# Performance work log

Hardware: AMD Instinct MI355X
Metric: run time of the kernel (lower is better)

## Reference

```python
import jax, jax.numpy as jnp
import numpy as np

NV, NK, DK, DV, KC = 32, 16, 128, 128, 4  # value heads, key heads, head dims, conv kernel
EPS = 1e-6


def setup_inputs() -> dict:
    key = jax.random.key(0)
    ks = jax.random.split(key, 10)
    B, T, D = 2, 4096, 2048
    key_dim, value_dim = NK * DK, NV * DV
    conv_dim = 2 * key_dim + value_dim
    s = 0.02
    return {
        "hidden_states": jax.random.normal(ks[0], (B, T, D), jnp.float32),
        "W_qkv": jax.random.normal(ks[1], (D, conv_dim), jnp.float32) * s,
        "W_z": jax.random.normal(ks[2], (D, value_dim), jnp.float32) * s,
        "W_b": jax.random.normal(ks[3], (D, NV), jnp.float32) * s,
        "W_a": jax.random.normal(ks[4], (D, NV), jnp.float32) * s,
        "conv_w": jax.random.normal(ks[5], (conv_dim, KC), jnp.float32) * 0.2,
        "dt_bias": jnp.ones((NV,), jnp.float32),
        "A_log": jnp.log(jax.random.uniform(ks[6], (NV,), jnp.float32, 0.5, 16.0)),
        "norm_w": jnp.ones((DV,), jnp.float32),
        "W_out": jax.random.normal(ks[7], (value_dim, D), jnp.float32) * s,
    }


def _silu(x):
    return x * jax.nn.sigmoid(x)


def _l2norm(x):
    return x * jax.lax.rsqrt(jnp.sum(x * x, axis=-1, keepdims=True) + EPS)


def _gated_delta_rule(q, k, v, g, beta):
    # q,k: [B,T,H,DK]; v: [B,T,H,DV]; g,beta: [B,T,H]
    tm = lambda x: jnp.moveaxis(x, 1, 0)  # time-major
    B, T, H = q.shape[0], q.shape[1], q.shape[2]
    S0 = jnp.zeros((B, H, q.shape[-1], v.shape[-1]), q.dtype)

    def step(S, xs):
        qt, kt, vt, gt, bt = xs
        S = S * jnp.exp(gt)[..., None, None]                       # decay
        kS = jnp.einsum('bhk,bhkv->bhv', kt, S)                    # k^T S
        S = S + bt[..., None, None] * kt[..., :, None] * (vt - kS)[..., None, :]
        o = jnp.einsum('bhk,bhkv->bhv', qt, S)
        return S, o

    _, o = jax.lax.scan(step, S0, (tm(q), tm(k), tm(v), tm(g), tm(beta)))
    return jnp.moveaxis(o, 0, 1)  # [B,T,H,DV]


def reference(hidden_states, W_qkv, W_z, W_b, W_a, conv_w, dt_bias, A_log, norm_w, W_out):
    B, T, D = hidden_states.shape
    key_dim, value_dim = NK * DK, NV * DV

    mixed = hidden_states @ W_qkv                                  # [B,T,conv_dim]
    z = (hidden_states @ W_z).reshape(B, T, NV, DV)
    beta = jax.nn.sigmoid(hidden_states @ W_b)                     # [B,T,NV]
    a = hidden_states @ W_a
    g = -jnp.exp(A_log) * jax.nn.softplus(a + dt_bias)             # [B,T,NV]

    # causal depthwise short conv (kernel KC) + silu
    xp = jnp.pad(mixed, ((0, 0), (KC - 1, 0), (0, 0)))
    conv = sum(xp[:, i:i + T, :] * conv_w[:, i] for i in range(KC))
    mixed = _silu(conv)

    q, k, v = jnp.split(mixed, [key_dim, 2 * key_dim], axis=-1)
    q = q.reshape(B, T, NK, DK)
    k = k.reshape(B, T, NK, DK)
    v = v.reshape(B, T, NV, DV)
    rep = NV // NK
    q = jnp.repeat(q, rep, axis=2)
    k = jnp.repeat(k, rep, axis=2)

    q = _l2norm(q) * (DK ** -0.5)
    k = _l2norm(k)

    o = _gated_delta_rule(q, k, v, g, beta)                        # [B,T,NV,DV]

    # fused gated RMSNorm: rmsnorm(o)*w * silu(z)
    var = jnp.mean(o * o, axis=-1, keepdims=True)
    o = o * jax.lax.rsqrt(var + 1e-6) * norm_w * _silu(z)

    return o.reshape(B, T, value_dim) @ W_out
```

## Files before the change

### kernel.cpp

```cpp
#include <hip/hip_runtime.h>
#include <hip/hip_bf16.h>


typedef __attribute__((ext_vector_type(8))) short short8;
typedef __attribute__((ext_vector_type(4))) float f32x4;
typedef unsigned short us;

static __device__ __forceinline__ us f2b(float f) {
  __hip_bfloat16 h = __float2bfloat16(f);
  return __builtin_bit_cast(us, h);
}
static __device__ __forceinline__ float b2f(us u) {
  return __bfloat162float(__builtin_bit_cast(__hip_bfloat16, u));
}
static __device__ __forceinline__ void bar_lds() {
  asm volatile("s_waitcnt lgkmcnt(0)" ::: "memory");
  __builtin_amdgcn_s_barrier();
}

__global__ __launch_bounds__(256) void cvt_f32_bf16(const float* __restrict__ in,
    us* __restrict__ out, long n4) {
  long i = (long)blockIdx.x * 256 + threadIdx.x;
  long stride = (long)gridDim.x * 256;
  for (; i < n4; i += stride) {
    float4 f = reinterpret_cast<const float4*>(in)[i];
    ushort4 u;
    u.x = f2b(f.x); u.y = f2b(f.y); u.z = f2b(f.z); u.w = f2b(f.w);
    reinterpret_cast<ushort4*>(out)[i] = u;
  }
}

__global__ __launch_bounds__(256) void transpose_cvt(const float* __restrict__ in,
    us* __restrict__ out, int K, int N, int Nfull, int coloff, int row_off) {
  __shared__ float tile[64][65];
  int tid = threadIdx.x;
  int n0 = blockIdx.x * 64, k0 = blockIdx.y * 64;
  int tx = tid & 15, ty = tid >> 4;
#pragma unroll
  for (int r = 0; r < 4; ++r) {
    int kk = k0 + ty + r * 16, nn = n0 + tx * 4;
    float4 v = make_float4(0.f, 0.f, 0.f, 0.f);
    if (kk < K && nn < N)
      v = *reinterpret_cast<const float4*>(in + (size_t)kk * Nfull + coloff + nn);
    tile[ty + r * 16][tx * 4 + 0] = v.x;
    tile[ty + r * 16][tx * 4 + 1] = v.y;
    tile[ty + r * 16][tx * 4 + 2] = v.z;
    tile[ty + r * 16][tx * 4 + 3] = v.w;
  }
  __syncthreads();
#pragma unroll
  for (int g = 0; g < 2; ++g) {
    int s = tid + g * 256;
    int nn = s >> 3, ks = (s & 7) * 8;
    if (n0 + nn < N && k0 + ks < K) {
      us ov[8];
#pragma unroll
      for (int i = 0; i < 8; ++i) ov[i] = f2b(tile[ks + i][nn]);
      *reinterpret_cast<uint4*>(out + (size_t)(n0 + nn + row_off) * K + k0 + ks) =
          *reinterpret_cast<uint4*>(ov);
    }
  }
}

template <bool BF16OUT>
__global__ __launch_bounds__(512, 1) void gemm256(const us* __restrict__ A,
    const us* __restrict__ B, void* __restrict__ Cout, int K, int ldC) {
  __shared__ us Abuf[2][256 * 64];
  __shared__ us Bbuf[2][256 * 64];
  int tid = threadIdx.x, w = tid >> 6, lane = tid & 63;
  int wr = w >> 2, wc = w & 3;
  int fr = lane & 15, j4 = lane >> 4;
  int lin = blockIdx.y * gridDim.x + blockIdx.x;
  int nwg = gridDim.x * gridDim.y;
  int wg = (lin & 7) * (nwg >> 3) + (lin >> 3);
  int bx = wg % gridDim.x, by = wg / gridDim.x;
  size_t bm = (size_t)bx * 256, bn = (size_t)by * 256;

  const us *aG[4], *bG[4];
  us *aL[2][4], *bL[2][4];
#pragma unroll
  for (int u = 0; u < 4; ++u) {
    int idx = u * 512 + tid;
    int row = idx >> 3, sl = idx & 7;
    int sg = (sl ^ (row & 7)) * 8;
    aG[u] = A + (bm + row) * K + sg;
    bG[u] = B + (bn + row) * K + sg;
    int lbase = (u * 64 + w * 8) * 64;
#pragma unroll
    for (int bf = 0; bf < 2; ++bf) {
      aL[bf][u] = &Abuf[bf][lbase];
      bL[bf][u] = &Bbuf[bf][lbase];
    }
  }

  f32x4 acc[8][4] = {};
#pragma unroll
  for (int u = 0; u < 4; ++u) {
    __builtin_amdgcn_global_load_lds((const void*)aG[u], (void*)aL[0][u], 16, 0, 0);
    __builtin_amdgcn_global_load_lds((const void*)bG[u], (void*)bL[0][u], 16, 0, 0);
  }
  __syncthreads();

  int nt = K >> 6;
  for (int t = 0; t < nt; ++t) {
    int cur = t & 1, nxt = cur ^ 1;
    const us* Ac = Abuf[cur];
    const us* Bc = Bbuf[cur];
    int kt1 = (t + 1) << 6;
    bool more = (t + 1 < nt);
#pragma unroll
    for (int q = 0; q < 4; ++q) {
      if (more) {
        __builtin_amdgcn_global_load_lds((const void*)(aG[q] + kt1), (void*)aL[nxt][q], 16, 0, 0);
        __builtin_amdgcn_global_load_lds((const void*)(bG[q] + kt1), (void*)bL[nxt][q], 16, 0, 0);
      }
      short8 a0[2], a1[2], bfv[4][2];
      int Ra0 = wr * 128 + 2 * q * 16 + fr;
      int Ra1 = Ra0 + 16;
#pragma unroll
      for (int ks = 0; ks < 2; ++ks) {
        a0[ks] = *reinterpret_cast<const short8*>(&Ac[Ra0 * 64 + (((ks * 4 + j4) ^ (Ra0 & 7)) * 8)]);
        a1[ks] = *reinterpret_cast<const short8*>(&Ac[Ra1 * 64 + (((ks * 4 + j4) ^ (Ra1 & 7)) * 8)]);
#pragma unroll
        for (int fj = 0; fj < 4; ++fj) {
          int Rb = wc * 64 + fj * 16 + fr;
          bfv[fj][ks] = *reinterpret_cast<const short8*>(&Bc[Rb * 64 + (((ks * 4 + j4) ^ (Rb & 7)) * 8)]);
        }
      }
      __builtin_amdgcn_s_setprio(1);
#pragma unroll
      for (int ks = 0; ks < 2; ++ks)
#pragma unroll
        for (int fj = 0; fj < 4; ++fj) {
          acc[2 * q][fj] = __builtin_amdgcn_mfma_f32_16x16x32_bf16(a0[ks], bfv[fj][ks], acc[2 * q][fj], 0, 0, 0);
          acc[2 * q + 1][fj] = __builtin_amdgcn_mfma_f32_16x16x32_bf16(a1[ks], bfv[fj][ks], acc[2 * q + 1][fj], 0, 0, 0);
        }
      __builtin_amdgcn_s_setprio(0);
    }
    __syncthreads();
  }
#pragma unroll
  for (int fi = 0; fi < 8; ++fi)
#pragma unroll
    for (int fj = 0; fj < 4; ++fj) {
      size_t col = bn + wc * 64 + fj * 16 + fr;
#pragma unroll
      for (int e = 0; e < 4; ++e) {
        size_t r = bm + wr * 128 + fi * 16 + j4 * 4 + e;
        size_t off = r * ldC + col;
        if (BF16OUT) reinterpret_cast<us*>(Cout)[off] = f2b(acc[fi][fj][e]);
        else reinterpret_cast<float*>(Cout)[off] = acc[fi][fj][e];
      }
    }
}

__global__ __launch_bounds__(256) void gemm_lds_f32(const us* __restrict__ A,
    const us* __restrict__ B, float* __restrict__ Cout,
    int K, int Nb1, int Nvalid, int ldC) {
  __shared__ us Ash[128 * 64];
  __shared__ us Bsh[128 * 64];
  int tid = threadIdx.x, w = tid >> 6, lane = tid & 63;
  int bm = blockIdx.x * 128, bn = blockIdx.y * 128;
  int wm = (w >> 1) * 64, wn = (w & 1) * 64;
  const us* aP[4]; const us* bP[4]; us* lA[4]; us* lB[4];
#pragma unroll
  for (int i = 0; i < 4; ++i) {
    int idx = i * 256 + tid;
    int row = idx >> 3;
    int sg = ((idx & 7) ^ (row & 7)) * 8;
    aP[i] = A + (size_t)(bm + row) * K + sg;
    int rb = bn + row; if (rb > Nb1) rb = Nb1;
    bP[i] = B + (size_t)rb * K + sg;
    lA[i] = &Ash[(i * 256 + w * 64) * 8];
    lB[i] = &Bsh[(i * 256 + w * 64) * 8];
  }
  f32x4 acc[4][4] = {};
  int fr = lane & 15, j = lane >> 4;
  for (int kt = 0; kt < K; kt += 64) {
#pragma unroll
    for (int i = 0; i < 4; ++i)
      __builtin_amdgcn_global_load_lds((const void*)(aP[i] + kt), (void*)lA[i], 16, 0, 0);
#pragma unroll
    for (int i = 0; i < 4; ++i)
      __builtin_amdgcn_global_load_lds((const void*)(bP[i] + kt), (void*)lB[i], 16, 0, 0);
    __syncthreads();
#pragma unroll
    for (int ks = 0; ks < 2; ++ks) {
      short8 af[4], bfr[4];
#pragma unroll
      for (int f = 0; f < 4; ++f) {
        int Ra = wm + f * 16 + fr;
        af[f] = *reinterpret_cast<const short8*>(&Ash[Ra * 64 + (((ks * 4 + j) ^ (Ra & 7)) * 8)]);
        int Rb = wn + f * 16 + fr;
        bfr[f] = *reinterpret_cast<const short8*>(&Bsh[Rb * 64 + (((ks * 4 + j) ^ (Rb & 7)) * 8)]);
      }
#pragma unroll
      for (int i = 0; i < 4; ++i)
#pragma unroll
        for (int jj = 0; jj < 4; ++jj)
          acc[i][jj] = __builtin_amdgcn_mfma_f32_16x16x32_bf16(af[i], bfr[jj], acc[i][jj], 0, 0, 0);
    }
    __syncthreads();
  }
#pragma unroll
  for (int i = 0; i < 4; ++i)
#pragma unroll
    for (int jj = 0; jj < 4; ++jj) {
      int c0 = bn + wn + jj * 16 + (lane & 15);
      if (c0 < Nvalid) {
#pragma unroll
        for (int e = 0; e < 4; ++e) {
          int r = bm + wm + i * 16 + (lane >> 4) * 4 + e;
          Cout[(size_t)r * ldC + c0] = acc[i][jj][e];
        }
      }
    }
}

template <int MODE>
__global__ __launch_bounds__(256) void conv_chunk(const us* __restrict__ mixed,
    const float* __restrict__ cw, us* __restrict__ outp, int headbase) {
  int bp = blockIdx.x, b = bp >> 11, tloc = (bp & 2047) * 2, tid = threadIdx.x;
  int c0 = tid * 8;
  float wv[8][4];
#pragma unroll
  for (int jj = 0; jj < 8; ++jj) {
    float4 w4 = *reinterpret_cast<const float4*>(cw + (size_t)(c0 + jj) * 4);
    wv[jj][0] = w4.x; wv[jj][1] = w4.y; wv[jj][2] = w4.z; wv[jj][3] = w4.w;
  }
  us rw[5][8];
#pragma unroll
  for (int i = 0; i < 5; ++i) {
    int tt = tloc - 3 + i;
    if (tt >= 0)
      *reinterpret_cast<uint4*>(rw[i]) = *reinterpret_cast<const uint4*>(
          mixed + ((size_t)(b * 4096 + tt)) * 2048 + c0);
    else
      *reinterpret_cast<uint4*>(rw[i]) = make_uint4(0, 0, 0, 0);
  }
  float x0[8], x1[8];
#pragma unroll
  for (int jj = 0; jj < 8; ++jj) {
    float a0 = 0.f, a1 = 0.f;
#pragma unroll
    for (int i = 0; i < 4; ++i) {
      a0 += b2f(rw[i][jj]) * wv[jj][i];
      a1 += b2f(rw[i + 1][jj]) * wv[jj][i];
    }
    x0[jj] = a0 / (1.f + __expf(-a0));
    x1[jj] = a1 / (1.f + __expf(-a1));
  }
  size_t bt0 = (size_t)b * 4096 + tloc;
  us ov[8];
  if (MODE < 2) {
    float s0 = 0.f, s1 = 0.f;
#pragma unroll
    for (int jj = 0; jj < 8; ++jj) { s0 += x0[jj] * x0[jj]; s1 += x1[jj] * x1[jj]; }
#pragma unroll
    for (int m = 1; m < 16; m <<= 1) {
      s0 += __shfl_xor(s0, m, 64);
      s1 += __shfl_xor(s1, m, 64);
    }
    const float sc = (MODE == 0 ? 0.08838834764831845f : 1.f);
    float rn0 = rsqrtf(s0 + 1e-6f) * sc;
    float rn1 = rsqrtf(s1 + 1e-6f) * sc;
    int head = tid >> 4, d0 = c0 & 127;
#pragma unroll
    for (int jj = 0; jj < 8; ++jj) ov[jj] = f2b(x0[jj] * rn0);
    *reinterpret_cast<uint4*>(outp + (bt0 * 16 + head) * 128 + d0) =
        *reinterpret_cast<uint4*>(ov);
#pragma unroll
    for (int jj = 0; jj < 8; ++jj) ov[jj] = f2b(x1[jj] * rn1);
    *reinterpret_cast<uint4*>(outp + ((bt0 + 1) * 16 + head) * 128 + d0) =
        *reinterpret_cast<uint4*>(ov);
  } else {
    int head = headbase + (c0 >> 7), d0 = c0 & 127;
#pragma unroll
    for (int jj = 0; jj < 8; ++jj) ov[jj] = f2b(x0[jj]);
    *reinterpret_cast<uint4*>(outp + (bt0 * 32 + head) * 128 + d0) =
        *reinterpret_cast<uint4*>(ov);
#pragma unroll
    for (int jj = 0; jj < 8; ++jj) ov[jj] = f2b(x1[jj]);
    *reinterpret_cast<uint4*>(outp + ((bt0 + 1) * 32 + head) * 128 + d0) =
        *reinterpret_cast<uint4*>(ov);
  }
}

__global__ __launch_bounds__(256) void gates_cumsum(const float* __restrict__ ba,
    const float* __restrict__ dt_bias, const float* __restrict__ A_log,
    float* __restrict__ bl_g, float* __restrict__ beta_g) {
  int widx = blockIdx.x * 4 + (threadIdx.x >> 6);
  int lane = threadIdx.x & 63;
  int bh = widx >> 6, chunk = widx & 63;
  int b = bh >> 5, h = bh & 31;
  size_t btl = (size_t)b * 4096 + chunk * 64 + lane;
  float bv = ba[btl * 64 + h];
  float av = ba[btl * 64 + 32 + h];
  float beta = 1.f / (1.f + __expf(-bv));
  float xx = av + dt_bias[h];
  float sp = (xx > 20.f) ? xx : log1pf(__expf(xx));
  float g = -__expf(A_log[h]) * sp;
#pragma unroll
  for (int off = 1; off < 64; off <<= 1) {
    float n = __shfl_up(g, off, 64);
    if (lane >= off) g += n;
  }
  bl_g[(size_t)widx * 64 + lane] = g;
  beta_g[(size_t)widx * 64 + lane] = beta;
}

static __device__ __forceinline__ f32x4 tile_range(const us* A, int lda,
    const us* B, int ldb, int rt, int ct, int l0, int nk, int lane, f32x4 acc) {
  const us* ar = A + (rt * 16 + (lane & 15)) * lda + l0 * 16 + (lane >> 4) * 8;
  const us* br = B + (ct * 16 + (lane & 15)) * ldb + l0 * 16 + (lane >> 4) * 8;
#pragma unroll
  for (int ks = 0; ks < nk; ++ks) {
    short8 a = *reinterpret_cast<const short8*>(ar + ks * 32);
    short8 bb = *reinterpret_cast<const short8*>(br + ks * 32);
    acc = __builtin_amdgcn_mfma_f32_16x16x32_bf16(a, bb, acc, 0, 0, 0);
  }
  return acc;
}
template <int SA, int SB>
static __device__ __forceinline__ f32x4 tile_swz(const us* A, int lda,
    const us* B, int ldb, int rt, int ct, int nk, int lane, f32x4 acc) {
  int ra = rt * 16 + (lane & 15);
  int rb = ct * 16 + (lane & 15);
  int j = lane >> 4;
#pragma unroll
  for (int ks = 0; ks < nk; ++ks) {
    int slot = j + 4 * ks;
    int oa = (SA >= 0) ? ((slot ^ ((ra >> SA) & 7)) * 8) : (slot * 8);
    int ob = (SB >= 0) ? ((slot ^ ((rb >> SB) & 7)) * 8) : (slot * 8);
    short8 a = *reinterpret_cast<const short8*>(A + ra * lda + oa);
    short8 bb = *reinterpret_cast<const short8*>(B + rb * ldb + ob);
    acc = __builtin_amdgcn_mfma_f32_16x16x32_bf16(a, bb, acc, 0, 0, 0);
  }
  return acc;
}

__global__ __launch_bounds__(512, 1) void scan_p1(
    const us* __restrict__ k, const float* __restrict__ bl_g,
    const float* __restrict__ beta_g, us* __restrict__ Tg) {
  __shared__ us Kb[64 * 136];
  __shared__ us Ebt[64 * 72];
  __shared__ us W1[64 * 72], W1t[64 * 72], W3[64 * 72];
  __shared__ float bl_s[64], bet_s[64];
  us* const Eb = Kb;

  int bid = blockIdx.x, bh = bid >> 6, c = bid & 63;
  int b = bh >> 5, h = bh & 31, hk = h >> 1;
  int tid = threadIdx.x, w = tid >> 6, lane = tid & 63;
  int row = tid >> 3, c16 = (tid & 7) * 16;
  size_t bt0 = (size_t)b * 4096 + c * 64;

  const int TR_[10] = {0, 1, 1, 2, 2, 2, 3, 3, 3, 3};
  const int TC_[10] = {0, 0, 1, 0, 1, 2, 0, 1, 2, 3};

  const us* kp = k + ((bt0 + row) * 16 + hk) * 128 + c16;
  uint4 kr0 = reinterpret_cast<const uint4*>(kp)[0];
  uint4 kr1 = reinterpret_cast<const uint4*>(kp)[1];
  int gbase = (bh * 64 + c) * 64;
  if (tid < 64) { bl_s[tid] = bl_g[gbase + tid]; bet_s[tid] = beta_g[gbase + tid]; }
  *reinterpret_cast<uint4*>(&Kb[row * 136 + c16]) = kr0;
  *reinterpret_cast<uint4*>(&Kb[row * 136 + c16 + 8]) = kr1;
  __syncthreads();
  {
    int art = w & 3;
#pragma unroll
    for (int s = 0; s < 2; ++s) {
      int ct = (w >> 2) * 2 + s;
      f32x4 a = tile_range(Kb, 136, Kb, 136, art, ct, 0, 4, lane, f32x4{});
#pragma unroll
      for (int e = 0; e < 4; ++e) {
        int tr = art * 16 + (lane >> 4) * 4 + e;
        int cl = ct * 16 + (lane & 15);
        float dv = (cl < tr) ? bet_s[tr] * __expf(bl_s[tr] - bl_s[cl]) * a[e] : 0.f;
        W1[tr * 72 + cl] = f2b(dv);
        W1t[cl * 72 + tr] = f2b(dv);
        W3[tr * 72 + cl] = f2b((tr == cl ? 1.f : 0.f) - dv);
      }
    }
  }
  __syncthreads();
  f32x4 freg[2] = {};
#pragma unroll
  for (int it = 1; it <= 5; ++it) {
    if (it > 1) {
#pragma unroll
      for (int s = 0; s < 2; ++s) {
        int j = w + s * 8;
        if (j < 10) {
          int r = TR_[j], cc0 = TC_[j];
#pragma unroll
          for (int e = 0; e < 4; ++e) {
            int rr = r * 16 + (lane >> 4) * 4 + e, cl = cc0 * 16 + (lane & 15);
            W3[rr * 72 + cl] = f2b(b2f(W3[rr * 72 + cl]) + freg[s][e]);
          }
        }
      }
    }
    if (it == 1) {
      const int ZR[12] = {0, 0, 0, 1, 1, 2, 1, 2, 2, 3, 3, 3};
      const int ZC[12] = {1, 2, 3, 2, 3, 3, 0, 0, 1, 0, 1, 2};
#pragma unroll
      for (int u = 0; u < 12; ++u) {
        if ((u & 7) != w) continue;
        us* arr = (u < 6) ? Eb : Ebt;
        if (lane < 32) {
          int rr = ZR[u] * 16 + (lane >> 1);
          *reinterpret_cast<uint4*>(&arr[rr * 72 + ZC[u] * 16 + (lane & 1) * 8]) =
              make_uint4(0, 0, 0, 0);
        }
      }
    }
    const us* Es  = (it & 1) ? W1  : Eb;
    const us* Est = (it & 1) ? W1t : Ebt;
    us* Ed  = (it & 1) ? Eb  : W1;
    us* Edt = (it & 1) ? Ebt : W1t;
#pragma unroll
    for (int s = 0; s < 2; ++s) {
      int j = w + s * 8;
      if (j < 10) {
        int r = TR_[j], cc0 = TC_[j];
        int l0 = cc0 & ~1, nk = (r - l0 + 2) >> 1;
        f32x4 a = tile_range(Es, 72, Est, 72, r, cc0, l0, nk, lane, f32x4{});
#pragma unroll
        for (int e = 0; e < 4; ++e) {
          int rr = r * 16 + (lane >> 4) * 4 + e, cl = cc0 * 16 + (lane & 15);
          us val = f2b(a[e]);
          Ed[rr * 72 + cl] = val;
          Edt[cl * 72 + rr] = val;
        }
      }
    }
    __syncthreads();
    const us* Ent = (it & 1) ? Ebt : W1t;
#pragma unroll
    for (int s = 0; s < 2; ++s) {
      int j = w + s * 8;
      if (j < 10) {
        int r = TR_[j], cc0 = TC_[j];
        int l0 = cc0 & ~1, nk = (r - l0 + 2) >> 1;
        freg[s] = tile_range(W3, 72, Ent, 72, r, cc0, l0, nk, lane, f32x4{});
      }
    }
    __syncthreads();
  }
#pragma unroll
  for (int s = 0; s < 2; ++s) {
    int j = w + s * 8;
    if (j < 10) {
      int r = TR_[j], cc0 = TC_[j];
#pragma unroll
      for (int e = 0; e < 4; ++e) {
        int rr = r * 16 + (lane >> 4) * 4 + e, cl = cc0 * 16 + (lane & 15);
        W3[rr * 72 + cl] = f2b(b2f(W3[rr * 72 + cl]) + freg[s][e]);
      }
    }
  }
  __syncthreads();
  *reinterpret_cast<uint4*>(&Tg[(size_t)bid * 4096 + tid * 8]) =
      *reinterpret_cast<const uint4*>(&W3[row * 72 + (tid & 7) * 8]);
}

__global__ __launch_bounds__(512, 1) void scan_p2(
    const us* __restrict__ q, const us* __restrict__ k, const us* __restrict__ v,
    const float* __restrict__ bl_g, const float* __restrict__ beta_g,
    const us* __restrict__ Tg, us* __restrict__ o) {
  __shared__ us Sb[32 * 136];
  __shared__ us Kb[64 * 136];
  __shared__ us Qb[64 * 136];
  __shared__ us Ktb[128 * 72];
  __shared__ us Vt[32 * 72];
  __shared__ us Ut[32 * 72];
  __shared__ us W3[64 * 72];
  __shared__ us WP[64 * 72];
  __shared__ float bl_s[64], bet_s[64], ksc_s[64];

  int bid = blockIdx.x, vs = bid >> 6, bh = bid & 63;
  int b = bh >> 5, h = bh & 31, hk = h >> 1;
  int tid = threadIdx.x, w = tid >> 6, lane = tid & 63;
  int row = tid >> 3, c16 = (tid & 7) * 16;

  for (int i = tid; i < (32 * 136) / 8; i += 512)
    reinterpret_cast<uint4*>(Sb)[i] = make_uint4(0, 0, 0, 0);
  __syncthreads();

  uint4 kr0, kr1, qr0, qr1, vr, Tr;
  float blr, blC, bet, betv;
  int vrow = (tid & 255) >> 2, vseg = tid & 3;
  auto load_regs = [&](int c) {
    size_t bt0 = (size_t)b * 4096 + c * 64;
    const us* kp = k + ((bt0 + row) * 16 + hk) * 128 + c16;
    const us* qp = q + ((bt0 + row) * 16 + hk) * 128 + c16;
    kr0 = reinterpret_cast<const uint4*>(kp)[0];
    kr1 = reinterpret_cast<const uint4*>(kp)[1];
    qr0 = reinterpret_cast<const uint4*>(qp)[0];
    qr1 = reinterpret_cast<const uint4*>(qp)[1];
    Tr = *reinterpret_cast<const uint4*>(&Tg[((size_t)bh * 64 + c) * 4096 + tid * 8]);
    int gbase = (bh * 64 + c) * 64;
    blr = bl_g[gbase + row];
    blC = bl_g[gbase + 63];
    bet = beta_g[gbase + row];
    if (tid < 256) {
      vr = *reinterpret_cast<const uint4*>(
          v + ((bt0 + vrow) * 32 + h) * 128 + vs * 32 + vseg * 8);
      betv = beta_g[gbase + vrow];
    }
  };
  load_regs(0);

  for (int c = 0; c < 64; ++c) {
    size_t bt0 = (size_t)b * 4096 + c * 64;
    if ((tid & 7) == 0) {
      bl_s[row] = blr; bet_s[row] = bet;
      ksc_s[row] = __expf(blC - blr);
    }
    *reinterpret_cast<uint4*>(&Kb[row * 136 + c16]) = kr0;
    *reinterpret_cast<uint4*>(&Kb[row * 136 + c16 + 8]) = kr1;
    *reinterpret_cast<uint4*>(&Qb[row * 136 + c16]) = qr0;
    *reinterpret_cast<uint4*>(&Qb[row * 136 + c16 + 8]) = qr1;
    *reinterpret_cast<uint4*>(&W3[row * 72 + (tid & 7) * 8]) = Tr;
    if (tid < 256) {
      us vreg[8];
      *reinterpret_cast<uint4*>(vreg) = vr;
#pragma unroll
      for (int i = 0; i < 8; ++i) {
        int vv = vseg * 8 + i;
        Vt[vv * 72 + (((vrow >> 3) ^ vseg) & 7) * 8 + (vrow & 7)] = f2b(betv * b2f(vreg[i]));
      }
    }
    load_regs(c < 63 ? c + 1 : 63);
    bar_lds();
#pragma unroll
    for (int tk = 0; tk < 2; ++tk) {
      int task = tid + tk * 512;
      int d = task & 127, oct = task >> 7;
      us kt[8];
#pragma unroll
      for (int i = 0; i < 8; ++i)
        kt[i] = f2b(ksc_s[oct * 8 + i] * b2f(Kb[(oct * 8 + i) * 136 + d]));
      *reinterpret_cast<uint4*>(&Ktb[d * 72 + ((oct ^ ((d >> 4) & 7)) * 8)]) =
          *reinterpret_cast<uint4*>(kt);
    }
    int rtO = w >> 1, ctv = w & 1;
    f32x4 o1 = tile_swz<-1, -1>(Qb, 136, Sb, 136, rtO, ctv, 4, lane, f32x4{});
    {
      int art = w & 3;
#pragma unroll
      for (int s = 0; s < 2; ++s) {
        int ct = (w >> 2) * 2 + s;
        f32x4 a = tile_swz<-1, -1>(Qb, 136, Kb, 136, art, ct, 4, lane, f32x4{});
#pragma unroll
        for (int e = 0; e < 4; ++e) {
          int tr = art * 16 + (lane >> 4) * 4 + e;
          int cl = ct * 16 + (lane & 15);
          float pv = (cl <= tr) ? __expf(bl_s[tr] - bl_s[cl]) * a[e] : 0.f;
          WP[tr * 72 + cl] = f2b(pv);
        }
      }
    }
    {
      int vrt = w >> 2, ct = w & 3;
      f32x4 a = tile_swz<-1, -1>(Sb, 136, Kb, 136, vrt, ct, 4, lane, f32x4{});
      int tt = ct * 16 + (lane & 15);
      float csc = bet_s[tt] * __expf(bl_s[tt]);
#pragma unroll
      for (int e = 0; e < 4; ++e) {
        int vv = vrt * 16 + (lane >> 4) * 4 + e;
        int off = vv * 72 + (((tt >> 3) ^ ((vv >> 3) & 7)) * 8) + (tt & 7);
        Vt[off] = f2b(b2f(Vt[off]) - csc * a[e]);
      }
    }
    bar_lds();
    {
      int vrt = w >> 2, ct = w & 3;
      f32x4 a = tile_swz<3, -1>(Vt, 72, W3, 72, vrt, ct, 2, lane, f32x4{});
#pragma unroll
      for (int e = 0; e < 4; ++e) {
        int uv = vrt * 16 + (lane >> 4) * 4 + e;
        int ut2 = ct * 16 + (lane & 15);
        Ut[uv * 72 + (((ut2 >> 3) ^ ((uv >> 3) & 7)) * 8) + (ut2 & 7)] = f2b(a[e]);
      }
    }
    bar_lds();
    float lamC = __expf(bl_s[63]);
    {
      f32x4 a = tile_swz<-1, 3>(WP, 72, Ut, 72, rtO, ctv, 2, lane, f32x4{});
#pragma unroll
      for (int e = 0; e < 4; ++e) {
        int tt = rtO * 16 + (lane >> 4) * 4 + e;
        int vv = vs * 32 + ctv * 16 + (lane & 15);
        float val = __expf(bl_s[tt]) * o1[e] + a[e];
        o[((bt0 + tt) * 32 + h) * 128 + vv] = f2b(val);
      }
    }
#pragma unroll
    for (int s = 0; s < 2; ++s) {
      int ti = w * 2 + s;
      int vrt = ti >> 3, dt = ti & 7;
      f32x4 a = tile_swz<3, 4>(Ut, 72, Ktb, 72, vrt, dt, 2, lane, f32x4{});
#pragma unroll
      for (int e = 0; e < 4; ++e) {
        int vv = vrt * 16 + (lane >> 4) * 4 + e, dd = dt * 16 + (lane & 15);
        Sb[vv * 136 + dd] = f2b(lamC * b2f(Sb[vv * 136 + dd]) + a[e]);
      }
    }
    bar_lds();
  }
}

__global__ __launch_bounds__(256) void rms_gate(us* oy,
    const us* __restrict__ z, const float* __restrict__ nw) {
  int sub = threadIdx.x & 31;
  size_t row = (size_t)blockIdx.x * 8 + (threadIdx.x >> 5);
  size_t base = row * 128 + sub * 4;
  ushort4 ov = *reinterpret_cast<ushort4*>(oy + base);
  ushort4 zv = *reinterpret_cast<const ushort4*>(z + base);
  float o_[4] = {b2f(ov.x), b2f(ov.y), b2f(ov.z), b2f(ov.w)};
  float ss = o_[0] * o_[0] + o_[1] * o_[1] + o_[2] * o_[2] + o_[3] * o_[3];
#pragma unroll
  for (int m = 1; m < 32; m <<= 1) ss += __shfl_xor(ss, m, 64);
  float r = rsqrtf(ss * (1.f / 128.f) + 1e-6f);
  float4 w4 = *reinterpret_cast<const float4*>(nw + sub * 4);
  float zz[4] = {b2f(zv.x), b2f(zv.y), b2f(zv.z), b2f(zv.w)};
  float wv[4] = {w4.x, w4.y, w4.z, w4.w};
  us res[4];
#pragma unroll
  for (int i = 0; i < 4; ++i) {
    float zs = zz[i] / (1.f + __expf(-zz[i]));
    res[i] = f2b(o_[i] * r * wv[i] * zs);
  }
  *reinterpret_cast<ushort4*>(oy + base) = *reinterpret_cast<ushort4*>(res);
}

extern "C" void kernel_launch(void* const* d_in, const int* in_sizes, int n_in,
                              void* d_out, int out_size, void* d_ws, size_t ws_size,
                              hipStream_t stream) {
  const float* hs      = (const float*)d_in[0];
  const float* W_qkv   = (const float*)d_in[1];
  const float* W_z     = (const float*)d_in[2];
  const float* W_b     = (const float*)d_in[3];
  const float* W_a     = (const float*)d_in[4];
  const float* conv_w  = (const float*)d_in[5];
  const float* dt_bias = (const float*)d_in[6];
  const float* A_log   = (const float*)d_in[7];
  const float* norm_w  = (const float*)d_in[8];
  const float* W_out   = (const float*)d_in[9];
  float* out = (float*)d_out;

  char* ws = (char*)d_ws;
  const size_t MiB = 1u << 20;
  float* ba_buf = (float*)(ws);
  float* bl_g   = (float*)(ws + 2 * MiB);
  float* bt_g   = (float*)(ws + 3 * MiB);
  us*    wt     = (us*)(ws + 4 * MiB);
  us*    Tg     = (us*)(ws + 4 * MiB);
  us*    mixed  = (us*)(ws + 36 * MiB);
  us*    o_buf  = (us*)(ws + 36 * MiB);
  us*    hs_bf0 = (us*)(ws + 68 * MiB);
  us*    q_buf  = (us*)(ws + 100 * MiB);
  us*    hs_bf1 = q_buf;
  us*    k_buf  = (us*)(ws + 132 * MiB);
  us*    v_buf  = (us*)(ws + 164 * MiB);
  us*    z_bf   = v_buf;

  cvt_f32_bf16<<<2048, 256, 0, stream>>>(hs, hs_bf0, (long)8192 * 2048 / 4);

  for (int c = 0; c < 4; ++c) {
    transpose_cvt<<<dim3(32, 32), 256, 0, stream>>>(W_qkv, wt, 2048, 2048, 8192, c * 2048, 0);
    gemm256<true><<<dim3(32, 8), 512, 0, stream>>>(hs_bf0, wt, mixed, 2048, 2048);
    const float* cwc = conv_w + (size_t)c * 2048 * 4;
    if (c == 0)      conv_chunk<0><<<4096, 256, 0, stream>>>(mixed, cwc, q_buf, 0);
    else if (c == 1) conv_chunk<1><<<4096, 256, 0, stream>>>(mixed, cwc, k_buf, 0);
    else if (c == 2) conv_chunk<2><<<4096, 256, 0, stream>>>(mixed, cwc, v_buf, 0);
    else             conv_chunk<2><<<4096, 256, 0, stream>>>(mixed, cwc, v_buf, 16);
  }
  transpose_cvt<<<dim3(1, 32), 256, 0, stream>>>(W_b, wt, 2048, 32, 32, 0, 0);
  transpose_cvt<<<dim3(1, 32), 256, 0, stream>>>(W_a, wt, 2048, 32, 32, 0, 32);
  gemm_lds_f32<<<dim3(64, 1), 256, 0, stream>>>(hs_bf0, wt, ba_buf, 2048, 63, 64, 64);
  gates_cumsum<<<1024, 256, 0, stream>>>(ba_buf, dt_bias, A_log, bl_g, bt_g);
  scan_p1<<<4096, 512, 0, stream>>>(k_buf, bl_g, bt_g, Tg);
  scan_p2<<<256, 512, 0, stream>>>(q_buf, k_buf, v_buf, bl_g, bt_g, Tg, o_buf);
  cvt_f32_bf16<<<2048, 256, 0, stream>>>(hs, hs_bf1, (long)8192 * 2048 / 4);
  transpose_cvt<<<dim3(64, 32), 256, 0, stream>>>(W_z, wt, 2048, 4096, 4096, 0, 0);
  gemm256<true><<<dim3(32, 16), 512, 0, stream>>>(hs_bf1, wt, z_bf, 2048, 4096);
  rms_gate<<<32768, 256, 0, stream>>>(o_buf, z_bf, norm_w);
  transpose_cvt<<<dim3(32, 64), 256, 0, stream>>>(W_out, wt, 4096, 2048, 2048, 0, 0);
  gemm256<false><<<dim3(32, 8), 512, 0, stream>>>(o_buf, wt, out, 4096, 2048);
}
```

Before: 1.081 ms.

## Halve GEMM K-tile to 32 and process four timesteps per conv block

The bf16 GEMM now stages 32-wide K slices instead of 64, which halves its LDS footprint. It uses a new XOR swizzle and spreads the single global-to-LDS load per matrix half across the four q sub-iterations. The conv+silu+l2norm kernel now handles four timesteps per block instead of two, so the overlapping history rows are reused across more outputs and the launch uses half as many blocks. The GEMM change doubles the number of K-loop iterations and barriers, and each barrier now covers less MFMA work.

```diff
diff --git a/kernel.cpp b/kernel.cpp
--- a/kernel.cpp
+++ b/kernel.cpp
@@ -65,8 +65,8 @@
 template <bool BF16OUT>
 __global__ __launch_bounds__(512, 1) void gemm256(const us* __restrict__ A,
     const us* __restrict__ B, void* __restrict__ Cout, int K, int ldC) {
-  __shared__ us Abuf[2][256 * 64];
-  __shared__ us Bbuf[2][256 * 64];
+  __shared__ us Abuf[2][256 * 32];
+  __shared__ us Bbuf[2][256 * 32];
   int tid = threadIdx.x, w = tid >> 6, lane = tid & 63;
   int wr = w >> 2, wc = w & 3;
   int fr = lane & 15, j4 = lane >> 4;
@@ -76,16 +76,16 @@
   int bx = wg % gridDim.x, by = wg / gridDim.x;
   size_t bm = (size_t)bx * 256, bn = (size_t)by * 256;
 
-  const us *aG[4], *bG[4];
-  us *aL[2][4], *bL[2][4];
-#pragma unroll
-  for (int u = 0; u < 4; ++u) {
+  const us *aG[2], *bG[2];
+  us *aL[2][2], *bL[2][2];
+#pragma unroll
+  for (int u = 0; u < 2; ++u) {
     int idx = u * 512 + tid;
-    int row = idx >> 3, sl = idx & 7;
-    int sg = (sl ^ (row & 7)) * 8;
+    int row = idx >> 2, sl = idx & 3;
+    int sg = (sl ^ ((row >> 1) & 3)) * 8;
     aG[u] = A + (bm + row) * K + sg;
     bG[u] = B + (bn + row) * K + sg;
-    int lbase = (u * 64 + w * 8) * 64;
+    int lbase = (u * 128 + w * 16) * 32;
 #pragma unroll
     for (int bf = 0; bf < 2; ++bf) {
       aL[bf][u] = &Abuf[bf][lbase];
@@ -95,46 +95,47 @@
 
   f32x4 acc[8][4] = {};
 #pragma unroll
-  for (int u = 0; u < 4; ++u) {
+  for (int u = 0; u < 2; ++u) {
     __builtin_amdgcn_global_load_lds((const void*)aG[u], (void*)aL[0][u], 16, 0, 0);
     __builtin_amdgcn_global_load_lds((const void*)bG[u], (void*)bL[0][u], 16, 0, 0);
   }
   __syncthreads();
 
-  int nt = K >> 6;
+  int nt = K >> 5;
   for (int t = 0; t < nt; ++t) {
     int cur = t & 1, nxt = cur ^ 1;
     const us* Ac = Abuf[cur];
     const us* Bc = Bbuf[cur];
-    int kt1 = (t + 1) << 6;
+    int kt1 = (t + 1) << 5;
     bool more = (t + 1 < nt);
 #pragma unroll
     for (int q = 0; q < 4; ++q) {
       if (more) {
-        __builtin_amdgcn_global_load_lds((const void*)(aG[q] + kt1), (void*)aL[nxt][q], 16, 0, 0);
-        __builtin_amdgcn_global_load_lds((const void*)(bG[q] + kt1), (void*)bL[nxt][q], 16, 0, 0);
-      }
-      short8 a0[2], a1[2], bfv[4][2];
+        if (q == 0)
+          __builtin_amdgcn_global_load_lds((const void*)(aG[0] + kt1), (void*)aL[nxt][0], 16, 0, 0);
+        else if (q == 1)
+          __builtin_amdgcn_global_load_lds((const void*)(aG[1] + kt1), (void*)aL[nxt][1], 16, 0, 0);
+        else if (q == 2)
+          __builtin_amdgcn_global_load_lds((const void*)(bG[0] + kt1), (void*)bL[nxt][0], 16, 0, 0);
+        else
+          __builtin_amdgcn_global_load_lds((const void*)(bG[1] + kt1), (void*)bL[nxt][1], 16, 0, 0);
+      }
+      short8 a0, a1, bfv[4];
       int Ra0 = wr * 128 + 2 * q * 16 + fr;
       int Ra1 = Ra0 + 16;
-#pragma unroll
-      for (int ks = 0; ks < 2; ++ks) {
-        a0[ks] = *reinterpret_cast<const short8*>(&Ac[Ra0 * 64 + (((ks * 4 + j4) ^ (Ra0 & 7)) * 8)]);
-        a1[ks] = *reinterpret_cast<const short8*>(&Ac[Ra1 * 64 + (((ks * 4 + j4) ^ (Ra1 & 7)) * 8)]);
-#pragma unroll
-        for (int fj = 0; fj < 4; ++fj) {
-          int Rb = wc * 64 + fj * 16 + fr;
-          bfv[fj][ks] = *reinterpret_cast<const short8*>(&Bc[Rb * 64 + (((ks * 4 + j4) ^ (Rb & 7)) * 8)]);
-        }
+      a0 = *reinterpret_cast<const short8*>(&Ac[Ra0 * 32 + ((j4 ^ ((Ra0 >> 1) & 3)) * 8)]);
+      a1 = *reinterpret_cast<const short8*>(&Ac[Ra1 * 32 + ((j4 ^ ((Ra1 >> 1) & 3)) * 8)]);
+#pragma unroll
+      for (int fj = 0; fj < 4; ++fj) {
+        int Rb = wc * 64 + fj * 16 + fr;
+        bfv[fj] = *reinterpret_cast<const short8*>(&Bc[Rb * 32 + ((j4 ^ ((Rb >> 1) & 3)) * 8)]);
       }
       __builtin_amdgcn_s_setprio(1);
 #pragma unroll
-      for (int ks = 0; ks < 2; ++ks)
-#pragma unroll
-        for (int fj = 0; fj < 4; ++fj) {
-          acc[2 * q][fj] = __builtin_amdgcn_mfma_f32_16x16x32_bf16(a0[ks], bfv[fj][ks], acc[2 * q][fj], 0, 0, 0);
-          acc[2 * q + 1][fj] = __builtin_amdgcn_mfma_f32_16x16x32_bf16(a1[ks], bfv[fj][ks], acc[2 * q + 1][fj], 0, 0, 0);
-        }
+      for (int fj = 0; fj < 4; ++fj) {
+        acc[2 * q][fj] = __builtin_amdgcn_mfma_f32_16x16x32_bf16(a0, bfv[fj], acc[2 * q][fj], 0, 0, 0);
+        acc[2 * q + 1][fj] = __builtin_amdgcn_mfma_f32_16x16x32_bf16(a1, bfv[fj], acc[2 * q + 1][fj], 0, 0, 0);
+      }
       __builtin_amdgcn_s_setprio(0);
     }
     __syncthreads();
@@ -220,7 +221,7 @@
 template <int MODE>
 __global__ __launch_bounds__(256) void conv_chunk(const us* __restrict__ mixed,
     const float* __restrict__ cw, us* __restrict__ outp, int headbase) {
-  int bp = blockIdx.x, b = bp >> 11, tloc = (bp & 2047) * 2, tid = threadIdx.x;
+  int bp = blockIdx.x, b = bp >> 10, tloc = (bp & 1023) * 4, tid = threadIdx.x;
   int c0 = tid * 8;
   float wv[8][4];
 #pragma unroll
@@ -228,61 +229,60 @@
     float4 w4 = *reinterpret_cast<const float4*>(cw + (size_t)(c0 + jj) * 4);
     wv[jj][0] = w4.x; wv[jj][1] = w4.y; wv[jj][2] = w4.z; wv[jj][3] = w4.w;
   }
-  us rw[5][8];
-#pragma unroll
-  for (int i = 0; i < 5; ++i) {
+  us rw[7][8];
+#pragma unroll
+  for (int i = 0; i < 7; ++i) {
     int tt = tloc - 3 + i;
-    if (tt >= 0)
+    if (tt >= 0 && tt < 4096)
       *reinterpret_cast<uint4*>(rw[i]) = *reinterpret_cast<const uint4*>(
           mixed + ((size_t)(b * 4096 + tt)) * 2048 + c0);
     else
       *reinterpret_cast<uint4*>(rw[i]) = make_uint4(0, 0, 0, 0);
   }
-  float x0[8], x1[8];
+  float x[4][8];
 #pragma unroll
   for (int jj = 0; jj < 8; ++jj) {
-    float a0 = 0.f, a1 = 0.f;
-#pragma unroll
-    for (int i = 0; i < 4; ++i) {
-      a0 += b2f(rw[i][jj]) * wv[jj][i];
-      a1 += b2f(rw[i + 1][jj]) * wv[jj][i];
-    }
-    x0[jj] = a0 / (1.f + __expf(-a0));
-    x1[jj] = a1 / (1.f + __expf(-a1));
+#pragma unroll
+    for (int tk = 0; tk < 4; ++tk) {
+      float a = 0.f;
+#pragma unroll
+      for (int i = 0; i < 4; ++i) a += b2f(rw[tk + i][jj]) * wv[jj][i];
+      x[tk][jj] = a / (1.f + __expf(-a));
+    }
   }
   size_t bt0 = (size_t)b * 4096 + tloc;
   us ov[8];
   if (MODE < 2) {
-    float s0 = 0.f, s1 = 0.f;
-#pragma unroll
-    for (int jj = 0; jj < 8; ++jj) { s0 += x0[jj] * x0[jj]; s1 += x1[jj] * x1[jj]; }
+    float s[4] = {};
+#pragma unroll
+    for (int tk = 0; tk < 4; ++tk) {
+#pragma unroll
+      for (int jj = 0; jj < 8; ++jj) s[tk] += x[tk][jj] * x[tk][jj];
+    }
 #pragma unroll
     for (int m = 1; m < 16; m <<= 1) {
-      s0 += __shfl_xor(s0, m, 64);
-      s1 += __shfl_xor(s1, m, 64);
+#pragma unroll
+      for (int tk = 0; tk < 4; ++tk) s[tk] += __shfl_xor(s[tk], m, 64);
     }
     const float sc = (MODE == 0 ? 0.08838834764831845f : 1.f);
-    float rn0 = rsqrtf(s0 + 1e-6f) * sc;
-    float rn1 = rsqrtf(s1 + 1e-6f) * sc;
     int head = tid >> 4, d0 = c0 & 127;
 #pragma unroll
-    for (int jj = 0; jj < 8; ++jj) ov[jj] = f2b(x0[jj] * rn0);
-    *reinterpret_cast<uint4*>(outp + (bt0 * 16 + head) * 128 + d0) =
-        *reinterpret_cast<uint4*>(ov);
-#pragma unroll
-    for (int jj = 0; jj < 8; ++jj) ov[jj] = f2b(x1[jj] * rn1);
-    *reinterpret_cast<uint4*>(outp + ((bt0 + 1) * 16 + head) * 128 + d0) =
-        *reinterpret_cast<uint4*>(ov);
+    for (int tk = 0; tk < 4; ++tk) {
+      float rn = rsqrtf(s[tk] + 1e-6f) * sc;
+#pragma unroll
+      for (int jj = 0; jj < 8; ++jj) ov[jj] = f2b(x[tk][jj] * rn);
+      *reinterpret_cast<uint4*>(outp + ((bt0 + tk) * 16 + head) * 128 + d0) =
+          *reinterpret_cast<uint4*>(ov);
+    }
   } else {
     int head = headbase + (c0 >> 7), d0 = c0 & 127;
 #pragma unroll
-    for (int jj = 0; jj < 8; ++jj) ov[jj] = f2b(x0[jj]);
-    *reinterpret_cast<uint4*>(outp + (bt0 * 32 + head) * 128 + d0) =
-        *reinterpret_cast<uint4*>(ov);
-#pragma unroll
-    for (int jj = 0; jj < 8; ++jj) ov[jj] = f2b(x1[jj]);
-    *reinterpret_cast<uint4*>(outp + ((bt0 + 1) * 32 + head) * 128 + d0) =
-        *reinterpret_cast<uint4*>(ov);
+    for (int tk = 0; tk < 4; ++tk) {
+#pragma unroll
+      for (int jj = 0; jj < 8; ++jj) ov[jj] = f2b(x[tk][jj]);
+      *reinterpret_cast<uint4*>(outp + ((bt0 + tk) * 32 + head) * 128 + d0) =
+          *reinterpret_cast<uint4*>(ov);
+    }
   }
 }
 
@@ -672,10 +672,10 @@
     transpose_cvt<<<dim3(32, 32), 256, 0, stream>>>(W_qkv, wt, 2048, 2048, 8192, c * 2048, 0);
     gemm256<true><<<dim3(32, 8), 512, 0, stream>>>(hs_bf0, wt, mixed, 2048, 2048);
     const float* cwc = conv_w + (size_t)c * 2048 * 4;
-    if (c == 0)      conv_chunk<0><<<4096, 256, 0, stream>>>(mixed, cwc, q_buf, 0);
-    else if (c == 1) conv_chunk<1><<<4096, 256, 0, stream>>>(mixed, cwc, k_buf, 0);
-    else if (c == 2) conv_chunk<2><<<4096, 256, 0, stream>>>(mixed, cwc, v_buf, 0);
-    else             conv_chunk<2><<<4096, 256, 0, stream>>>(mixed, cwc, v_buf, 16);
+    if (c == 0)      conv_chunk<0><<<2048, 256, 0, stream>>>(mixed, cwc, q_buf, 0);
+    else if (c == 1) conv_chunk<1><<<2048, 256, 0, stream>>>(mixed, cwc, k_buf, 0);
+    else if (c == 2) conv_chunk<2><<<2048, 256, 0, stream>>>(mixed, cwc, v_buf, 0);
+    else             conv_chunk<2><<<2048, 256, 0, stream>>>(mixed, cwc, v_buf, 16);
   }
   transpose_cvt<<<dim3(1, 32), 256, 0, stream>>>(W_b, wt, 2048, 32, 32, 0, 0);
   transpose_cvt<<<dim3(1, 32), 256, 0, stream>>>(W_a, wt, 2048, 32, 32, 0, 32);
```

Result: slower. 1.236 ms (+14.3%).
